# Optimization experiments

Measured on AMD Instinct MI355X. Metric: run time of the kernel, lower is better.

The kernel has to match this reference:

```python
import jax, jax.numpy as jnp
import numpy as np
import math

B, LQ, LK, D, H = 4, 1024, 1024, 1024, 16
DK = D // H
SCALE = 1.0 / math.sqrt(DK)
NEG_INF = -1.0e9


def setup_inputs() -> dict:
    key = jax.random.key(0)
    ks = jax.random.split(key, 18)
    w = lambda k: (jax.random.normal(k, (D, D), dtype=jnp.float32) * 0.02)
    b = lambda k: (jax.random.normal(k, (D,), dtype=jnp.float32) * 0.02)
    mask = jax.random.randint(ks[4], (B, 1, LK), 0, 2).astype(jnp.int32)
    mask = mask.at[..., 0].set(1)  # ensure at least one valid key per row
    return {
        "query": jax.random.normal(ks[0], (B, LQ, D), dtype=jnp.float32),
        "key": jax.random.normal(ks[1], (B, LK, D), dtype=jnp.float32),
        "value": jax.random.normal(ks[2], (B, LK, D), dtype=jnp.float32),
        "weak_rela": jax.random.normal(ks[3], (B, LK, D), dtype=jnp.float32),
        "mask": mask,
        "Wq": w(ks[5]), "bq": b(ks[6]),
        "Wk": w(ks[7]), "bk": b(ks[8]),
        "Wv": w(ks[9]), "bv": b(ks[10]),
        "Wrk": w(ks[11]), "brk": b(ks[12]),
        "Wrv": w(ks[13]), "brv": b(ks[14]),
        "Wo": w(ks[15]), "bo": b(ks[16]),
    }


def _proj(x, W, bias):
    # x: [B, L, D] -> [B, H, L, DK]; torch Linear: y = x @ W.T + b
    y = x @ W.T + bias
    Bn, L, _ = y.shape
    return y.reshape(Bn, L, H, DK).transpose(0, 2, 1, 3)


def reference(query, key, value, weak_rela, mask,
              Wq, bq, Wk, bk, Wv, bv, Wrk, brk, Wrv, brv, Wo, bo):
    q = _proj(query, Wq, bq)        # [B,H,LQ,DK]
    k = _proj(key, Wk, bk)          # [B,H,LK,DK]
    v = _proj(value, Wv, bv)        # [B,H,LK,DK]
    rk = _proj(weak_rela, Wrk, brk) # [B,H,LK,DK]
    rv = _proj(weak_rela, Wrv, brv) # [B,H,LK,DK]

    qk = jnp.einsum('bhqd,bhkd->bhqk', q, k) * SCALE
    qr = jnp.einsum('bhqd,bhkd->bhqk', q, rk) * SCALE

    m = (mask[:, None, :, :] == 0)  # [B,1,1,LK] broadcast over heads/queries
    qk = jnp.where(m, NEG_INF, qk)
    qr = jnp.where(m, NEG_INF, qr)

    p_vis = jax.nn.softmax(qk, axis=-1)
    p_rel = jax.nn.softmax(qr, axis=-1)

    x = (jnp.einsum('bhqk,bhkd->bhqd', p_vis, v)
         + jnp.einsum('bhqk,bhkd->bhqd', p_rel, rv))  # [B,H,LQ,DK]
    x = x.transpose(0, 2, 1, 3).reshape(query.shape[0], -1, H * DK)
    return x @ Wo.T + bo
```

## Files before the change

kernel.cpp:

```cpp
#include <hip/hip_runtime.h>
#include <stdint.h>

#define NB 4
#define NH 16
#define DKH 64
#define DMODEL 1024
#define SEQ 1024
#define SCALE 0.125f
#define NEG_INF -1.0e9f
#define K2E 0.18033688011112042f

typedef __bf16 bf16_t;
typedef __bf16 bf16x8 __attribute__((ext_vector_type(8)));
typedef __bf16 bf16x4v __attribute__((ext_vector_type(4)));
typedef float f32x4 __attribute__((ext_vector_type(4)));

typedef const uint32_t __attribute__((address_space(1)))* gas_ptr;
typedef uint32_t __attribute__((address_space(3)))* las_ptr;

__device__ __forceinline__ void gload_lds16(const void* g, void* l) {
  __builtin_amdgcn_global_load_lds((gas_ptr)g, (las_ptr)l, 16, 0, 0);
}


__global__ void cvt_multi(const float* __restrict__ i0, const float* __restrict__ i1,
                          const float* __restrict__ i2, const float* __restrict__ i3,
                          const float* __restrict__ i4, const float* __restrict__ i5,
                          bf16_t* o0, bf16_t* o1, bf16_t* o2, bf16_t* o3, bf16_t* o4, bf16_t* o5,
                          int n) {
  const int t = blockIdx.y;
  const float* in = (t == 0) ? i0 : (t == 1) ? i1 : (t == 2) ? i2 : (t == 3) ? i3 : (t == 4) ? i4 : i5;
  bf16_t* out = (t == 0) ? o0 : (t == 1) ? o1 : (t == 2) ? o2 : (t == 3) ? o3 : (t == 4) ? o4 : o5;
  const int idx = (blockIdx.x * 256 + threadIdx.x) * 4;
  if (idx >= n) return;
  const float4 v = *(const float4*)(in + idx);
  bf16x4v p;
  p[0] = (bf16_t)v.x; p[1] = (bf16_t)v.y; p[2] = (bf16_t)v.z; p[3] = (bf16_t)v.w;
  *(bf16x4v*)(out + idx) = p;
}

#define NXE ((size_t)NB * SEQ * DMODEL)
#define NWE ((size_t)DMODEL * DMODEL)

template<int MODE>
__device__ __forceinline__ void gemm128_body(
    const bf16_t* __restrict__ A, const bf16_t* __restrict__ W,
    const float* __restrict__ bias, void* __restrict__ outp,
    int m0, int n0, bf16_t* As, bf16_t* Bs) {
  const int tid = threadIdx.x;
  const int lane = tid & 63;
  const int w = tid >> 6;
  const int wm = w >> 1, wn = w & 1;
  const int g = lane >> 4, c = lane & 15;
  const int lrow = lane >> 3;
  const int lcol = ((lane & 7) * 8) ^ ((lane >> 3) << 3);
  const int sc = (c & 7) << 3;

  f32x4 acc[4][4] = {};

  for (int kt = 0; kt < DMODEL; kt += 64) {
#pragma unroll
    for (int p = 0; p < 4; ++p) {
      const int row = w * 32 + p * 8;
      gload_lds16(A + (size_t)(m0 + row + lrow) * DMODEL + kt + lcol, &As[row * 64]);
      gload_lds16(W + (size_t)(n0 + row + lrow) * DMODEL + kt + lcol, &Bs[row * 64]);
    }
    __syncthreads();
    bf16x8 af[4][2], bfr[4][2];
#pragma unroll
    for (int i = 0; i < 4; ++i)
#pragma unroll
      for (int kk = 0; kk < 2; ++kk) {
        af[i][kk]  = *(const bf16x8*)&As[(wm * 64 + i * 16 + c) * 64 + ((kk * 32 + g * 8) ^ sc)];
        bfr[i][kk] = *(const bf16x8*)&Bs[(wn * 64 + i * 16 + c) * 64 + ((kk * 32 + g * 8) ^ sc)];
      }
#pragma unroll
    for (int i = 0; i < 4; ++i)
#pragma unroll
      for (int j = 0; j < 4; ++j) {
        acc[i][j] = __builtin_amdgcn_mfma_f32_16x16x32_bf16(af[i][0], bfr[j][0], acc[i][j], 0, 0, 0);
        acc[i][j] = __builtin_amdgcn_mfma_f32_16x16x32_bf16(af[i][1], bfr[j][1], acc[i][j], 0, 0, 0);
      }
    __syncthreads();
  }

  float bv4[4];
#pragma unroll
  for (int j = 0; j < 4; ++j) bv4[j] = bias[n0 + wn * 64 + j * 16 + c];

#pragma unroll
  for (int i = 0; i < 4; ++i) {
    const int mrow = m0 + wm * 64 + i * 16 + g * 4;
    const int b_ = mrow >> 10, l_ = mrow & 1023;
#pragma unroll
    for (int j = 0; j < 4; ++j) {
      const int n = n0 + wn * 64 + j * 16 + c;
      if (MODE == 2) {
        float* o = (float*)outp;
#pragma unroll
        for (int r = 0; r < 4; ++r)
          o[(size_t)(mrow + r) * DMODEL + n] = acc[i][j][r] + bv4[j];
      } else if (MODE == 0) {
        bf16_t* o = (bf16_t*)outp;
        const int h_ = n >> 6, dk_ = n & 63;
#pragma unroll
        for (int r = 0; r < 4; ++r)
          o[((size_t)(b_ * NH + h_) * SEQ + l_ + r) * DKH + dk_] =
              (bf16_t)(acc[i][j][r] + bv4[j]);
      } else {
        bf16_t* o = (bf16_t*)outp;
        const int h_ = n >> 6, dk_ = n & 63;
        bf16x4v pk;
#pragma unroll
        for (int r = 0; r < 4; ++r) pk[r] = (bf16_t)(acc[i][j][r] + bv4[j]);
        *(bf16x4v*)&o[((size_t)(b_ * NH + h_) * DKH + dk_) * SEQ + l_] = pk;
      }
    }
  }
}

__global__ void __launch_bounds__(256, 2)
proj_gemm(const bf16_t* __restrict__ Xbase, const bf16_t* __restrict__ Wbase,
          bf16_t* __restrict__ Obase,
          const float* __restrict__ b0, const float* __restrict__ b1,
          const float* __restrict__ b2, const float* __restrict__ b3,
          const float* __restrict__ b4) {
  __shared__ bf16_t As[128 * 64];
  __shared__ bf16_t Bs[128 * 64];
  const int bid = blockIdx.x;
  const int lid = (bid & 7) * 160 + (bid >> 3);
  const int seg = lid >> 8;
  const int rr = lid & 255;
  const int m0 = (rr >> 3) * 128, n0 = (rr & 7) * 128;

  const bf16_t* A = Xbase + (size_t)((seg < 3) ? seg : 3) * NXE;
  const bf16_t* W = Wbase + (size_t)seg * NWE;
  const int ooff = (seg == 0) ? 0 : (seg == 1) ? 1 : (seg == 2) ? 3 : (seg == 3) ? 2 : 4;
  bf16_t* out = Obase + (size_t)ooff * NXE;
  const float* bias = (seg == 0) ? b0 : (seg == 1) ? b1 : (seg == 2) ? b2 : (seg == 3) ? b3 : b4;

  if (seg == 2 || seg == 4) gemm128_body<1>(A, W, bias, out, m0, n0, As, Bs);
  else                      gemm128_body<0>(A, W, bias, out, m0, n0, As, Bs);
}

__global__ void __launch_bounds__(256, 2)
out_gemm(const bf16_t* __restrict__ A, const bf16_t* __restrict__ W,
         const float* __restrict__ bias, float* __restrict__ out) {
  __shared__ bf16_t As[128 * 64];
  __shared__ bf16_t Bs[128 * 64];
  const int bid = blockIdx.x;
  const int lid = (bid & 7) * 32 + (bid >> 3);
  const int m0 = (lid >> 3) * 128, n0 = (lid & 7) * 128;
  gemm128_body<2>(A, W, bias, out, m0, n0, As, Bs);
}

__global__ void __launch_bounds__(256, 2)
attn_kernel(const bf16_t* __restrict__ q, const bf16_t* __restrict__ k,
            const bf16_t* __restrict__ rk, const bf16_t* __restrict__ vT,
            const bf16_t* __restrict__ rvT, const int* __restrict__ mask,
            bf16_t* __restrict__ x) {
  __shared__ bf16_t Ks[64 * 64], RKs[64 * 64], Vs[64 * 64], RVs[64 * 64];
  __shared__ bf16_t Ps[8][16 * 64];

  const int tid = threadIdx.x;
  const int lane = tid & 63;
  const int w = tid >> 6;
  const int g = lane >> 4, c = lane & 15;
  const int sc = (c & 7) << 3;
  const int bid = blockIdx.x;
  const int lid = (bid & 7) * 128 + (bid >> 3);
  const int qt = lid & 15;
  const int bh = lid >> 4;
  const int b = bh >> 4, h = bh & 15;
  const int q0 = qt * 64;

  const bf16_t* qp = q + (size_t)bh * SEQ * DKH;
  const bf16_t* kp = k + (size_t)bh * SEQ * DKH;
  const bf16_t* rkp = rk + (size_t)bh * SEQ * DKH;
  const bf16_t* vp = vT + (size_t)bh * DKH * SEQ;
  const bf16_t* rvp = rvT + (size_t)bh * DKH * SEQ;
  const int* mp = mask + b * SEQ;
  const int lrow = lane >> 3;
  const int lcol = ((lane & 7) * 8) ^ ((lane >> 3) << 3);

  bf16_t* Pv = Ps[w * 2];
  bf16_t* Pr = Ps[w * 2 + 1];

  bf16x8 qf[2];
#pragma unroll
  for (int kk = 0; kk < 2; ++kk)
    qf[kk] = *(const bf16x8*)(qp + (size_t)(q0 + w * 16 + c) * DKH + kk * 32 + g * 8);

  f32x4 ov[4] = {}, orl[4] = {};
  float mv = NEG_INF, mr = NEG_INF, lv = 0.f, lr = 0.f;

  for (int t = 0; t < 16; ++t) {
    const int kv0 = t * 64;
    if (t) __syncthreads();
#pragma unroll
    for (int p = 0; p < 2; ++p) {
      const int row = w * 16 + p * 8;
      gload_lds16(kp  + (size_t)(kv0 + row + lrow) * DKH + lcol, &Ks[row * 64]);
      gload_lds16(rkp + (size_t)(kv0 + row + lrow) * DKH + lcol, &RKs[row * 64]);
      gload_lds16(vp  + (size_t)(row + lrow) * SEQ + kv0 + lcol, &Vs[row * 64]);
      gload_lds16(rvp + (size_t)(row + lrow) * SEQ + kv0 + lcol, &RVs[row * 64]);
    }
    __syncthreads();

    int4 mk4[4];
#pragma unroll
    for (int f = 0; f < 4; ++f) mk4[f] = *(const int4*)&mp[kv0 + f * 16 + g * 4];

    f32x4 sv[4], sr[4];
#pragma unroll
    for (int f = 0; f < 4; ++f) {
      const bf16x8 k0  = *(const bf16x8*)&Ks [(f * 16 + c) * 64 + ((g * 8) ^ sc)];
      const bf16x8 k1  = *(const bf16x8*)&Ks [(f * 16 + c) * 64 + ((32 + g * 8) ^ sc)];
      const bf16x8 rk0 = *(const bf16x8*)&RKs[(f * 16 + c) * 64 + ((g * 8) ^ sc)];
      const bf16x8 rk1 = *(const bf16x8*)&RKs[(f * 16 + c) * 64 + ((32 + g * 8) ^ sc)];
      f32x4 a = {0.f, 0.f, 0.f, 0.f};
      a = __builtin_amdgcn_mfma_f32_16x16x32_bf16(k0, qf[0], a, 0, 0, 0);
      a = __builtin_amdgcn_mfma_f32_16x16x32_bf16(k1, qf[1], a, 0, 0, 0);
      sv[f] = a;
      f32x4 ar = {0.f, 0.f, 0.f, 0.f};
      ar = __builtin_amdgcn_mfma_f32_16x16x32_bf16(rk0, qf[0], ar, 0, 0, 0);
      ar = __builtin_amdgcn_mfma_f32_16x16x32_bf16(rk1, qf[1], ar, 0, 0, 0);
      sr[f] = ar;
    }

#pragma unroll
    for (int f = 0; f < 4; ++f) {
      const int4 m4 = mk4[f];
      sv[f][0] = (m4.x == 0) ? NEG_INF : sv[f][0] * K2E;
      sv[f][1] = (m4.y == 0) ? NEG_INF : sv[f][1] * K2E;
      sv[f][2] = (m4.z == 0) ? NEG_INF : sv[f][2] * K2E;
      sv[f][3] = (m4.w == 0) ? NEG_INF : sv[f][3] * K2E;
      sr[f][0] = (m4.x == 0) ? NEG_INF : sr[f][0] * K2E;
      sr[f][1] = (m4.y == 0) ? NEG_INF : sr[f][1] * K2E;
      sr[f][2] = (m4.z == 0) ? NEG_INF : sr[f][2] * K2E;
      sr[f][3] = (m4.w == 0) ? NEG_INF : sr[f][3] * K2E;
    }

    {
      float tm = fmaxf(fmaxf(sv[0][0], sv[0][1]), fmaxf(sv[0][2], sv[0][3]));
#pragma unroll
      for (int f = 1; f < 4; ++f)
        tm = fmaxf(tm, fmaxf(fmaxf(sv[f][0], sv[f][1]), fmaxf(sv[f][2], sv[f][3])));
      tm = fmaxf(tm, __shfl_xor(tm, 16));
      tm = fmaxf(tm, __shfl_xor(tm, 32));
      const float mnew = fmaxf(mv, tm);
      const float sf = __builtin_amdgcn_exp2f(mv - mnew);
      mv = mnew;
      float pf = 0.f;
#pragma unroll
      for (int f = 0; f < 4; ++f) {
        bf16x4v pk;
#pragma unroll
        for (int r = 0; r < 4; ++r) {
          const float p = __builtin_amdgcn_exp2f(sv[f][r] - mnew);
          pf += p;
          pk[r] = (bf16_t)p;
        }
        *(bf16x4v*)&Pv[c * 64 + ((f * 16 + g * 4) ^ sc)] = pk;
      }
      lv = lv * sf + pf;
#pragma unroll
      for (int jd = 0; jd < 4; ++jd)
#pragma unroll
        for (int r = 0; r < 4; ++r) ov[jd][r] *= sf;
    }

    {
      float tm = fmaxf(fmaxf(sr[0][0], sr[0][1]), fmaxf(sr[0][2], sr[0][3]));
#pragma unroll
      for (int f = 1; f < 4; ++f)
        tm = fmaxf(tm, fmaxf(fmaxf(sr[f][0], sr[f][1]), fmaxf(sr[f][2], sr[f][3])));
      tm = fmaxf(tm, __shfl_xor(tm, 16));
      tm = fmaxf(tm, __shfl_xor(tm, 32));
      const float mnew = fmaxf(mr, tm);
      const float sf = __builtin_amdgcn_exp2f(mr - mnew);
      mr = mnew;
      float pf = 0.f;
#pragma unroll
      for (int f = 0; f < 4; ++f) {
        bf16x4v pk;
#pragma unroll
        for (int r = 0; r < 4; ++r) {
          const float p = __builtin_amdgcn_exp2f(sr[f][r] - mnew);
          pf += p;
          pk[r] = (bf16_t)p;
        }
        *(bf16x4v*)&Pr[c * 64 + ((f * 16 + g * 4) ^ sc)] = pk;
      }
      lr = lr * sf + pf;
#pragma unroll
      for (int jd = 0; jd < 4; ++jd)
#pragma unroll
        for (int r = 0; r < 4; ++r) orl[jd][r] *= sf;
    }

    const bf16x8 pav0 = *(const bf16x8*)&Pv[c * 64 + ((g * 8) ^ sc)];
    const bf16x8 pav1 = *(const bf16x8*)&Pv[c * 64 + ((32 + g * 8) ^ sc)];
    const bf16x8 par0 = *(const bf16x8*)&Pr[c * 64 + ((g * 8) ^ sc)];
    const bf16x8 par1 = *(const bf16x8*)&Pr[c * 64 + ((32 + g * 8) ^ sc)];
#pragma unroll
    for (int jd = 0; jd < 4; ++jd) {
      const bf16x8 v0  = *(const bf16x8*)&Vs [(jd * 16 + c) * 64 + ((g * 8) ^ sc)];
      const bf16x8 v1  = *(const bf16x8*)&Vs [(jd * 16 + c) * 64 + ((32 + g * 8) ^ sc)];
      ov[jd]  = __builtin_amdgcn_mfma_f32_16x16x32_bf16(v0, pav0, ov[jd], 0, 0, 0);
      ov[jd]  = __builtin_amdgcn_mfma_f32_16x16x32_bf16(v1, pav1, ov[jd], 0, 0, 0);
      const bf16x8 rv0 = *(const bf16x8*)&RVs[(jd * 16 + c) * 64 + ((g * 8) ^ sc)];
      const bf16x8 rv1 = *(const bf16x8*)&RVs[(jd * 16 + c) * 64 + ((32 + g * 8) ^ sc)];
      orl[jd] = __builtin_amdgcn_mfma_f32_16x16x32_bf16(rv0, par0, orl[jd], 0, 0, 0);
      orl[jd] = __builtin_amdgcn_mfma_f32_16x16x32_bf16(rv1, par1, orl[jd], 0, 0, 0);
    }
  }

  lv += __shfl_xor(lv, 16); lv += __shfl_xor(lv, 32);
  lr += __shfl_xor(lr, 16); lr += __shfl_xor(lr, 32);
  const float rlv = 1.0f / lv, rlr = 1.0f / lr;

  bf16_t* xb = x + (size_t)b * SEQ * DMODEL + (size_t)h * DKH;
  const int qrow = q0 + w * 16 + c;
#pragma unroll
  for (int jd = 0; jd < 4; ++jd) {
    bf16x4v pk;
#pragma unroll
    for (int r = 0; r < 4; ++r)
      pk[r] = (bf16_t)(ov[jd][r] * rlv + orl[jd][r] * rlr);
    *(bf16x4v*)&xb[(size_t)qrow * DMODEL + jd * 16 + g * 4] = pk;
  }
}

extern "C" void kernel_launch(void* const* d_in, const int* in_sizes, int n_in,
                              void* d_out, int out_size, void* d_ws, size_t ws_size,
                              hipStream_t stream) {
  (void)in_sizes; (void)n_in; (void)out_size; (void)ws_size;
  const float* query = (const float*)d_in[0];
  const float* key_  = (const float*)d_in[1];
  const float* value = (const float*)d_in[2];
  const float* weak  = (const float*)d_in[3];
  const int*   mask  = (const int*)d_in[4];
  const float* Wq  = (const float*)d_in[5];  const float* bq  = (const float*)d_in[6];
  const float* Wk  = (const float*)d_in[7];  const float* bk  = (const float*)d_in[8];
  const float* Wv  = (const float*)d_in[9];  const float* bv  = (const float*)d_in[10];
  const float* Wrk = (const float*)d_in[11]; const float* brk = (const float*)d_in[12];
  const float* Wrv = (const float*)d_in[13]; const float* brv = (const float*)d_in[14];
  const float* Wo  = (const float*)d_in[15]; const float* bo  = (const float*)d_in[16];

  char* ws = (char*)d_ws;
  size_t off = 0;
  auto alloc = [&](size_t bytes) {
    void* p = ws + off;
    off += (bytes + 255) & ~(size_t)255;
    return p;
  };
  const size_t SZ_X = NXE * sizeof(bf16_t);
  const size_t SZ_W = NWE * sizeof(bf16_t);

  bf16_t* Xq = (bf16_t*)alloc(SZ_X);
  bf16_t* Xk = (bf16_t*)alloc(SZ_X);
  bf16_t* Xv = (bf16_t*)alloc(SZ_X);
  bf16_t* Xr = (bf16_t*)alloc(SZ_X);
  bf16_t* Wqb  = (bf16_t*)alloc(SZ_W);
  bf16_t* Wkb  = (bf16_t*)alloc(SZ_W);
  bf16_t* Wvb  = (bf16_t*)alloc(SZ_W);
  bf16_t* Wrkb = (bf16_t*)alloc(SZ_W);
  bf16_t* Wrvb = (bf16_t*)alloc(SZ_W);
  bf16_t* Wob  = (bf16_t*)alloc(SZ_W);
  bf16_t* qh   = (bf16_t*)alloc(SZ_X);
  bf16_t* kh   = (bf16_t*)alloc(SZ_X);
  bf16_t* rkh  = (bf16_t*)alloc(SZ_X);
  bf16_t* vTh  = (bf16_t*)alloc(SZ_X);
  bf16_t* rvTh = (bf16_t*)alloc(SZ_X);
  bf16_t* xh   = (bf16_t*)alloc(SZ_X);
  (void)Xk; (void)Xv; (void)Xr; (void)Wkb; (void)Wvb; (void)Wrkb; (void)Wrvb;
  (void)kh; (void)rkh; (void)vTh; (void)rvTh;

  cvt_multi<<<dim3(4096, 4), 256, 0, stream>>>(query, key_, value, weak, nullptr, nullptr,
                                               Xq, Xk, Xv, Xr, nullptr, nullptr,
                                               NB * SEQ * DMODEL);
  cvt_multi<<<dim3(1024, 6), 256, 0, stream>>>(Wq, Wk, Wv, Wrk, Wrv, Wo,
                                               Wqb, Wkb, Wvb, Wrkb, Wrvb, Wob,
                                               DMODEL * DMODEL);

  proj_gemm<<<dim3(1280), 256, 0, stream>>>(Xq, Wqb, qh, bq, bk, bv, brk, brv);

  attn_kernel<<<dim3(1024), 256, 0, stream>>>(qh, kh, rkh, vTh, rvTh, mask, xh);

  out_gemm<<<dim3(256), 256, 0, stream>>>(xh, Wob, bo, (float*)d_out);
}
```

Before: 187.4 us.

## Process two 16-row query tiles per wave in attention to reuse K/V fragments

Each wave now handles 32 query rows (two 16-row sub-tiles), so a block covers 128 queries and the grid drops from 1024 to 512 blocks. K and V fragments loaded from LDS are reused across both sub-tiles, and the visual and relational streams run one after the other through a shared helper that reuses the same P scratch buffer. This halves the global K/V/RK/RV tile traffic per query and the LDS fragment reads per MFMA. The cost is more accumulator registers per thread and fewer blocks, which on a 256-CU part may leave some CUs underused or lower occupancy.

```diff
diff --git a/kernel.cpp b/kernel.cpp
--- a/kernel.cpp
+++ b/kernel.cpp
@@ -154,25 +154,109 @@
   gemm128_body<2>(A, W, bias, out, m0, n0, As, Bs);
 }
 
+__device__ __forceinline__ void attn_step(
+    const bf16_t* __restrict__ Kt, const bf16_t* __restrict__ Vt,
+    bf16_t* __restrict__ Pw, const bf16x8 (&qf)[2][2], const int4 (&mk)[4],
+    float (&m_s)[2], float (&l_s)[2], f32x4 (&o_s)[2][4], int lane) {
+  const int g = lane >> 4, c = lane & 15;
+  const int sc = (c & 7) << 3;
+
+  f32x4 s[2][4];
+  {
+    bf16x8 kfr[4][2];
+#pragma unroll
+    for (int f = 0; f < 4; ++f) {
+      kfr[f][0] = *(const bf16x8*)&Kt[(f * 16 + c) * 64 + ((g * 8) ^ sc)];
+      kfr[f][1] = *(const bf16x8*)&Kt[(f * 16 + c) * 64 + ((32 + g * 8) ^ sc)];
+    }
+#pragma unroll
+    for (int i = 0; i < 2; ++i)
+#pragma unroll
+      for (int f = 0; f < 4; ++f) {
+        f32x4 a = {0.f, 0.f, 0.f, 0.f};
+        a = __builtin_amdgcn_mfma_f32_16x16x32_bf16(kfr[f][0], qf[i][0], a, 0, 0, 0);
+        a = __builtin_amdgcn_mfma_f32_16x16x32_bf16(kfr[f][1], qf[i][1], a, 0, 0, 0);
+        s[i][f] = a;
+      }
+  }
+
+#pragma unroll
+  for (int i = 0; i < 2; ++i)
+#pragma unroll
+    for (int f = 0; f < 4; ++f) {
+      const int4 m4 = mk[f];
+      s[i][f][0] = (m4.x == 0) ? NEG_INF : s[i][f][0] * K2E;
+      s[i][f][1] = (m4.y == 0) ? NEG_INF : s[i][f][1] * K2E;
+      s[i][f][2] = (m4.z == 0) ? NEG_INF : s[i][f][2] * K2E;
+      s[i][f][3] = (m4.w == 0) ? NEG_INF : s[i][f][3] * K2E;
+    }
+
+#pragma unroll
+  for (int i = 0; i < 2; ++i) {
+    float tm = fmaxf(fmaxf(s[i][0][0], s[i][0][1]), fmaxf(s[i][0][2], s[i][0][3]));
+#pragma unroll
+    for (int f = 1; f < 4; ++f)
+      tm = fmaxf(tm, fmaxf(fmaxf(s[i][f][0], s[i][f][1]), fmaxf(s[i][f][2], s[i][f][3])));
+    tm = fmaxf(tm, __shfl_xor(tm, 16));
+    tm = fmaxf(tm, __shfl_xor(tm, 32));
+    const float mnew = fmaxf(m_s[i], tm);
+    const float sf = __builtin_amdgcn_exp2f(m_s[i] - mnew);
+    m_s[i] = mnew;
+    float pf = 0.f;
+#pragma unroll
+    for (int f = 0; f < 4; ++f) {
+      bf16x4v pk;
+#pragma unroll
+      for (int r = 0; r < 4; ++r) {
+        const float p = __builtin_amdgcn_exp2f(s[i][f][r] - mnew);
+        pf += p;
+        pk[r] = (bf16_t)p;
+      }
+      *(bf16x4v*)&Pw[i * 1024 + c * 64 + ((f * 16 + g * 4) ^ sc)] = pk;
+    }
+    l_s[i] = l_s[i] * sf + pf;
+#pragma unroll
+    for (int jd = 0; jd < 4; ++jd)
+#pragma unroll
+      for (int r = 0; r < 4; ++r) o_s[i][jd][r] *= sf;
+  }
+
+  bf16x8 pa[2][2];
+#pragma unroll
+  for (int i = 0; i < 2; ++i) {
+    pa[i][0] = *(const bf16x8*)&Pw[i * 1024 + c * 64 + ((g * 8) ^ sc)];
+    pa[i][1] = *(const bf16x8*)&Pw[i * 1024 + c * 64 + ((32 + g * 8) ^ sc)];
+  }
+#pragma unroll
+  for (int jd = 0; jd < 4; ++jd) {
+    const bf16x8 v0 = *(const bf16x8*)&Vt[(jd * 16 + c) * 64 + ((g * 8) ^ sc)];
+    const bf16x8 v1 = *(const bf16x8*)&Vt[(jd * 16 + c) * 64 + ((32 + g * 8) ^ sc)];
+#pragma unroll
+    for (int i = 0; i < 2; ++i) {
+      o_s[i][jd] = __builtin_amdgcn_mfma_f32_16x16x32_bf16(v0, pa[i][0], o_s[i][jd], 0, 0, 0);
+      o_s[i][jd] = __builtin_amdgcn_mfma_f32_16x16x32_bf16(v1, pa[i][1], o_s[i][jd], 0, 0, 0);
+    }
+  }
+}
+
 __global__ void __launch_bounds__(256, 2)
 attn_kernel(const bf16_t* __restrict__ q, const bf16_t* __restrict__ k,
             const bf16_t* __restrict__ rk, const bf16_t* __restrict__ vT,
             const bf16_t* __restrict__ rvT, const int* __restrict__ mask,
             bf16_t* __restrict__ x) {
   __shared__ bf16_t Ks[64 * 64], RKs[64 * 64], Vs[64 * 64], RVs[64 * 64];
-  __shared__ bf16_t Ps[8][16 * 64];
+  __shared__ bf16_t Ps[4][2][16 * 64];
 
   const int tid = threadIdx.x;
   const int lane = tid & 63;
   const int w = tid >> 6;
   const int g = lane >> 4, c = lane & 15;
-  const int sc = (c & 7) << 3;
   const int bid = blockIdx.x;
-  const int lid = (bid & 7) * 128 + (bid >> 3);
-  const int qt = lid & 15;
-  const int bh = lid >> 4;
+  const int lid = (bid & 7) * 64 + (bid >> 3);
+  const int qt = lid & 7;
+  const int bh = lid >> 3;
   const int b = bh >> 4, h = bh & 15;
-  const int q0 = qt * 64;
+  const int q0 = qt * 128;
 
   const bf16_t* qp = q + (size_t)bh * SEQ * DKH;
   const bf16_t* kp = k + (size_t)bh * SEQ * DKH;
@@ -183,16 +267,16 @@
   const int lrow = lane >> 3;
   const int lcol = ((lane & 7) * 8) ^ ((lane >> 3) << 3);
 
-  bf16_t* Pv = Ps[w * 2];
-  bf16_t* Pr = Ps[w * 2 + 1];
-
-  bf16x8 qf[2];
-#pragma unroll
-  for (int kk = 0; kk < 2; ++kk)
-    qf[kk] = *(const bf16x8*)(qp + (size_t)(q0 + w * 16 + c) * DKH + kk * 32 + g * 8);
-
-  f32x4 ov[4] = {}, orl[4] = {};
-  float mv = NEG_INF, mr = NEG_INF, lv = 0.f, lr = 0.f;
+  bf16x8 qf[2][2];
+#pragma unroll
+  for (int i = 0; i < 2; ++i)
+#pragma unroll
+    for (int kk = 0; kk < 2; ++kk)
+      qf[i][kk] = *(const bf16x8*)(qp + (size_t)(q0 + w * 32 + i * 16 + c) * DKH + kk * 32 + g * 8);
+
+  f32x4 ov[2][4] = {}, orl[2][4] = {};
+  float mv[2] = {NEG_INF, NEG_INF}, mr[2] = {NEG_INF, NEG_INF};
+  float lv[2] = {0.f, 0.f}, lr[2] = {0.f, 0.f};
 
   for (int t = 0; t < 16; ++t) {
     const int kv0 = t * 64;
@@ -211,124 +295,29 @@
 #pragma unroll
     for (int f = 0; f < 4; ++f) mk4[f] = *(const int4*)&mp[kv0 + f * 16 + g * 4];
 
-    f32x4 sv[4], sr[4];
-#pragma unroll
-    for (int f = 0; f < 4; ++f) {
-      const bf16x8 k0  = *(const bf16x8*)&Ks [(f * 16 + c) * 64 + ((g * 8) ^ sc)];
-      const bf16x8 k1  = *(const bf16x8*)&Ks [(f * 16 + c) * 64 + ((32 + g * 8) ^ sc)];
-      const bf16x8 rk0 = *(const bf16x8*)&RKs[(f * 16 + c) * 64 + ((g * 8) ^ sc)];
-      const bf16x8 rk1 = *(const bf16x8*)&RKs[(f * 16 + c) * 64 + ((32 + g * 8) ^ sc)];
-      f32x4 a = {0.f, 0.f, 0.f, 0.f};
-      a = __builtin_amdgcn_mfma_f32_16x16x32_bf16(k0, qf[0], a, 0, 0, 0);
-      a = __builtin_amdgcn_mfma_f32_16x16x32_bf16(k1, qf[1], a, 0, 0, 0);
-      sv[f] = a;
-      f32x4 ar = {0.f, 0.f, 0.f, 0.f};
-      ar = __builtin_amdgcn_mfma_f32_16x16x32_bf16(rk0, qf[0], ar, 0, 0, 0);
-      ar = __builtin_amdgcn_mfma_f32_16x16x32_bf16(rk1, qf[1], ar, 0, 0, 0);
-      sr[f] = ar;
-    }
-
-#pragma unroll
-    for (int f = 0; f < 4; ++f) {
-      const int4 m4 = mk4[f];
-      sv[f][0] = (m4.x == 0) ? NEG_INF : sv[f][0] * K2E;
-      sv[f][1] = (m4.y == 0) ? NEG_INF : sv[f][1] * K2E;
-      sv[f][2] = (m4.z == 0) ? NEG_INF : sv[f][2] * K2E;
-      sv[f][3] = (m4.w == 0) ? NEG_INF : sv[f][3] * K2E;
-      sr[f][0] = (m4.x == 0) ? NEG_INF : sr[f][0] * K2E;
-      sr[f][1] = (m4.y == 0) ? NEG_INF : sr[f][1] * K2E;
-      sr[f][2] = (m4.z == 0) ? NEG_INF : sr[f][2] * K2E;
-      sr[f][3] = (m4.w == 0) ? NEG_INF : sr[f][3] * K2E;
-    }
-
-    {
-      float tm = fmaxf(fmaxf(sv[0][0], sv[0][1]), fmaxf(sv[0][2], sv[0][3]));
-#pragma unroll
-      for (int f = 1; f < 4; ++f)
-        tm = fmaxf(tm, fmaxf(fmaxf(sv[f][0], sv[f][1]), fmaxf(sv[f][2], sv[f][3])));
-      tm = fmaxf(tm, __shfl_xor(tm, 16));
-      tm = fmaxf(tm, __shfl_xor(tm, 32));
-      const float mnew = fmaxf(mv, tm);
-      const float sf = __builtin_amdgcn_exp2f(mv - mnew);
-      mv = mnew;
-      float pf = 0.f;
-#pragma unroll
-      for (int f = 0; f < 4; ++f) {
-        bf16x4v pk;
-#pragma unroll
-        for (int r = 0; r < 4; ++r) {
-          const float p = __builtin_amdgcn_exp2f(sv[f][r] - mnew);
-          pf += p;
-          pk[r] = (bf16_t)p;
-        }
-        *(bf16x4v*)&Pv[c * 64 + ((f * 16 + g * 4) ^ sc)] = pk;
-      }
-      lv = lv * sf + pf;
-#pragma unroll
-      for (int jd = 0; jd < 4; ++jd)
-#pragma unroll
-        for (int r = 0; r < 4; ++r) ov[jd][r] *= sf;
-    }
-
-    {
-      float tm = fmaxf(fmaxf(sr[0][0], sr[0][1]), fmaxf(sr[0][2], sr[0][3]));
-#pragma unroll
-      for (int f = 1; f < 4; ++f)
-        tm = fmaxf(tm, fmaxf(fmaxf(sr[f][0], sr[f][1]), fmaxf(sr[f][2], sr[f][3])));
-      tm = fmaxf(tm, __shfl_xor(tm, 16));
-      tm = fmaxf(tm, __shfl_xor(tm, 32));
-      const float mnew = fmaxf(mr, tm);
-      const float sf = __builtin_amdgcn_exp2f(mr - mnew);
-      mr = mnew;
-      float pf = 0.f;
-#pragma unroll
-      for (int f = 0; f < 4; ++f) {
-        bf16x4v pk;
-#pragma unroll
-        for (int r = 0; r < 4; ++r) {
-          const float p = __builtin_amdgcn_exp2f(sr[f][r] - mnew);
-          pf += p;
-          pk[r] = (bf16_t)p;
-        }
-        *(bf16x4v*)&Pr[c * 64 + ((f * 16 + g * 4) ^ sc)] = pk;
-      }
-      lr = lr * sf + pf;
-#pragma unroll
-      for (int jd = 0; jd < 4; ++jd)
-#pragma unroll
-        for (int r = 0; r < 4; ++r) orl[jd][r] *= sf;
-    }
-
-    const bf16x8 pav0 = *(const bf16x8*)&Pv[c * 64 + ((g * 8) ^ sc)];
-    const bf16x8 pav1 = *(const bf16x8*)&Pv[c * 64 + ((32 + g * 8) ^ sc)];
-    const bf16x8 par0 = *(const bf16x8*)&Pr[c * 64 + ((g * 8) ^ sc)];
-    const bf16x8 par1 = *(const bf16x8*)&Pr[c * 64 + ((32 + g * 8) ^ sc)];
+    attn_step(Ks,  Vs,  &Ps[w][0][0], qf, mk4, mv, lv, ov,  lane);
+    attn_step(RKs, RVs, &Ps[w][0][0], qf, mk4, mr, lr, orl, lane);
+  }
+
+#pragma unroll
+  for (int i = 0; i < 2; ++i) {
+    lv[i] += __shfl_xor(lv[i], 16); lv[i] += __shfl_xor(lv[i], 32);
+    lr[i] += __shfl_xor(lr[i], 16); lr[i] += __shfl_xor(lr[i], 32);
+  }
+
+  bf16_t* xb = x + (size_t)b * SEQ * DMODEL + (size_t)h * DKH;
+#pragma unroll
+  for (int i = 0; i < 2; ++i) {
+    const float rlv = 1.0f / lv[i], rlr = 1.0f / lr[i];
+    const int qrow = q0 + w * 32 + i * 16 + c;
 #pragma unroll
     for (int jd = 0; jd < 4; ++jd) {
-      const bf16x8 v0  = *(const bf16x8*)&Vs [(jd * 16 + c) * 64 + ((g * 8) ^ sc)];
-      const bf16x8 v1  = *(const bf16x8*)&Vs [(jd * 16 + c) * 64 + ((32 + g * 8) ^ sc)];
-      ov[jd]  = __builtin_amdgcn_mfma_f32_16x16x32_bf16(v0, pav0, ov[jd], 0, 0, 0);
-      ov[jd]  = __builtin_amdgcn_mfma_f32_16x16x32_bf16(v1, pav1, ov[jd], 0, 0, 0);
-      const bf16x8 rv0 = *(const bf16x8*)&RVs[(jd * 16 + c) * 64 + ((g * 8) ^ sc)];
-      const bf16x8 rv1 = *(const bf16x8*)&RVs[(jd * 16 + c) * 64 + ((32 + g * 8) ^ sc)];
-      orl[jd] = __builtin_amdgcn_mfma_f32_16x16x32_bf16(rv0, par0, orl[jd], 0, 0, 0);
-      orl[jd] = __builtin_amdgcn_mfma_f32_16x16x32_bf16(rv1, par1, orl[jd], 0, 0, 0);
-    }
-  }
-
-  lv += __shfl_xor(lv, 16); lv += __shfl_xor(lv, 32);
-  lr += __shfl_xor(lr, 16); lr += __shfl_xor(lr, 32);
-  const float rlv = 1.0f / lv, rlr = 1.0f / lr;
-
-  bf16_t* xb = x + (size_t)b * SEQ * DMODEL + (size_t)h * DKH;
-  const int qrow = q0 + w * 16 + c;
-#pragma unroll
-  for (int jd = 0; jd < 4; ++jd) {
-    bf16x4v pk;
-#pragma unroll
-    for (int r = 0; r < 4; ++r)
-      pk[r] = (bf16_t)(ov[jd][r] * rlv + orl[jd][r] * rlr);
-    *(bf16x4v*)&xb[(size_t)qrow * DMODEL + jd * 16 + g * 4] = pk;
+      bf16x4v pk;
+#pragma unroll
+      for (int r = 0; r < 4; ++r)
+        pk[r] = (bf16_t)(ov[i][jd][r] * rlv + orl[i][jd][r] * rlr);
+      *(bf16x4v*)&xb[(size_t)qrow * DMODEL + jd * 16 + g * 4] = pk;
+    }
   }
 }
 
@@ -386,7 +375,7 @@
 
   proj_gemm<<<dim3(1280), 256, 0, stream>>>(Xq, Wqb, qh, bq, bk, bv, brk, brv);
 
-  attn_kernel<<<dim3(1024), 256, 0, stream>>>(qh, kh, rkh, vTh, rvTh, mask, xh);
+  attn_kernel<<<dim3(512), 256, 0, stream>>>(qh, kh, rkh, vTh, rvTh, mask, xh);
 
   out_gemm<<<dim3(256), 256, 0, stream>>>(xh, Wob, bo, (float*)d_out);
 }
```

Result: faster. 170.4 us (-9.1%).
